# Kernel tuning notes

Hardware: AMD Instinct MI355X
Metric: run time of the kernel (lower is better)

## Reference

```python
import jax, jax.numpy as jnp
import numpy as np

B, C = 8192, 1000
T_KD = 20.0   # KL_divergence temperature
T_TH = 2.0    # Threshold_weights5 temperature
ALPHA = 0.8   # dynamic weight scale


def setup_inputs() -> dict:
    key = jax.random.key(0)
    ks = jax.random.split(key, 7)
    d = {f"outputs{i+1}": jax.random.normal(ks[i], (B, C), jnp.float32) for i in range(5)}
    d["out_s"] = jax.random.normal(ks[5], (B, C), jnp.float32)
    d["targets"] = jax.random.randint(ks[6], (B,), 0, C)
    return d


def _margin(o, targets):
    # per-sample: top1 - top2 if the target class holds the max logit, else 0
    top2 = jax.lax.top_k(o, 2)[0]                                   # [B, 2]
    tgt = jnp.take_along_axis(o, targets[:, None], axis=1)[:, 0]    # [B]
    return jnp.where(tgt == top2[:, 0], top2[:, 0] - top2[:, 1], jnp.zeros_like(tgt))


def reference(outputs1, outputs2, outputs3, outputs4, outputs5, out_s, targets):
    teachers = jnp.stack([outputs1, outputs2, outputs3, outputs4, outputs5], 0)  # [5,B,C]
    mimic = teachers.mean(0)                                                      # [B,C]
    all6 = jnp.concatenate([teachers, mimic[None]], axis=0)                       # [6,B,C]

    # Threshold_weights5: confidence margins -> softmax over the 6 sources
    margins = jax.vmap(lambda o: _margin(o, targets))(all6)        # [6,B]
    out_threshold = jax.nn.softmax(margins / T_TH, axis=0)         # [6,B]
    max_preds = teachers.max()                                     # scalar

    # Calculate_dynamic_weights for each source
    tgt_logits = jnp.take_along_axis(all6, targets[None, :, None], axis=2)[..., 0]  # [6,B]
    w2 = ALPHA * tgt_logits / max_preds                            # [6,B]
    w1 = 1.0 - w2                                                  # [6,B]

    # CE loss (shared across sources) and KD cross-entropy per source
    log_p_s = jax.nn.log_softmax(out_s, axis=1)
    CE = -jnp.take_along_axis(log_p_s, targets[:, None], axis=1)[:, 0]             # [B]
    log_p_sT = jax.nn.log_softmax(out_s / T_KD, axis=1)                            # [B,C]
    p_t = jax.nn.softmax(all6 / T_KD, axis=2)                                      # [6,B,C]
    KD = -jnp.sum(p_t * log_p_sT[None], axis=2) * (T_KD * T_KD)                    # [6,B]

    loss_src = w1 * CE[None, :] + w2 * KD                          # [6,B]
    return jnp.mean(jnp.sum(out_threshold * loss_src, axis=0))
```

## Files before the change

kernel.cpp:

```cpp
#include <hip/hip_runtime.h>
#include <math.h>

#define NROWS 8192
#define NCOLS 1000
#define NB    4096
#define ROWSPB 2
#define NSLOT 64
#define NEGF  -1.0e30f


__device__ __forceinline__ unsigned encf(float x) {
    unsigned u = __float_as_uint(x);
    return (u & 0x80000000u) ? ~u : (u | 0x80000000u);
}
__device__ __forceinline__ float decf(unsigned e) {
    unsigned u = (e & 0x80000000u) ? (e ^ 0x80000000u) : ~e;
    return __uint_as_float(u);
}
__device__ __forceinline__ float pick4(const float* a, int k) {
    return k == 0 ? a[0] : (k == 1 ? a[1] : (k == 2 ? a[2] : a[3]));
}

__global__ __launch_bounds__(64, 4) void row_kernel(
    const float* __restrict__ p0, const float* __restrict__ p1,
    const float* __restrict__ p2, const float* __restrict__ p3,
    const float* __restrict__ p4, const float* __restrict__ p5,
    const int* __restrict__ targets,
    double* __restrict__ S1, double* __restrict__ S2, unsigned* __restrict__ MX)
{
    const int bid = blockIdx.x;
    const int l   = threadIdx.x;

    double accCE = 0.0, accS2 = 0.0;
    float  accMax = NEGF;

    #pragma unroll
    for (int it = 0; it < ROWSPB; ++it) {
        const int row = bid + it * NB;
        const int tgt = targets[row];
        const int t4  = tgt >> 2;
        const int lt  = t4 & 63;
        const int qt  = t4 >> 6;
        const int kt  = tgt & 3;

        float m1[6], m2[6], zs[6], ds[6];
        #pragma unroll
        for (int s = 0; s < 6; ++s) { m1[s] = NEGF; m2[s] = NEGF; zs[s] = 0.f; ds[s] = 0.f; }
        float z1 = 0.f, z20 = 0.f;
        float sg[7];
        #pragma unroll
        for (int s = 0; s < 7; ++s) sg[s] = 0.f;

        #pragma unroll
        for (int q = 0; q < 4; ++q) {
            const int  c4   = l + (q << 6);
            const bool ok   = (c4 < (NCOLS >> 2));
            const size_t base = (size_t)row * NCOLS + ((size_t)c4 << 2);

            float v[7][4];
            if (ok) {
                float4 x0 = *(const float4*)(p0 + base);
                float4 x1 = *(const float4*)(p1 + base);
                float4 x2 = *(const float4*)(p2 + base);
                float4 x3 = *(const float4*)(p3 + base);
                float4 x4 = *(const float4*)(p4 + base);
                float4 x5 = *(const float4*)(p5 + base);
                v[0][0]=x0.x; v[0][1]=x0.y; v[0][2]=x0.z; v[0][3]=x0.w;
                v[1][0]=x1.x; v[1][1]=x1.y; v[1][2]=x1.z; v[1][3]=x1.w;
                v[2][0]=x2.x; v[2][1]=x2.y; v[2][2]=x2.z; v[2][3]=x2.w;
                v[3][0]=x3.x; v[3][1]=x3.y; v[3][2]=x3.z; v[3][3]=x3.w;
                v[4][0]=x4.x; v[4][1]=x4.y; v[4][2]=x4.z; v[4][3]=x4.w;
                v[6][0]=x5.x; v[6][1]=x5.y; v[6][2]=x5.z; v[6][3]=x5.w;
                #pragma unroll
                for (int k = 0; k < 4; ++k)
                    v[5][k] = (v[0][k] + v[1][k] + v[2][k] + v[3][k] + v[4][k]) * 0.2f;
            } else {
                #pragma unroll
                for (int s = 0; s < 7; ++s)
                    #pragma unroll
                    for (int k = 0; k < 4; ++k) v[s][k] = NEGF;
            }

            #pragma unroll
            for (int s = 0; s < 6; ++s) {
                float a = v[s][0], b = v[s][1], c = v[s][2], d = v[s][3];
                float hi1 = fmaxf(a, b), lo1 = fminf(a, b);
                float hi2 = fmaxf(c, d), lo2 = fminf(c, d);
                float q1 = fmaxf(hi1, hi2);
                float q2 = fmaxf(fminf(hi1, hi2), fmaxf(lo1, lo2));
                float nm1 = fmaxf(m1[s], q1);
                float nm2 = fmaxf(fminf(m1[s], q1), fmaxf(m2[s], q2));
                m1[s] = nm1; m2[s] = nm2;
                float zz = 0.f, dot = 0.f;
                #pragma unroll
                for (int k = 0; k < 4; ++k) {
                    float e = __expf(v[s][k] * 0.05f);
                    zz += e; dot += e * v[6][k];
                }
                zs[s] += zz; ds[s] += dot;
            }
            #pragma unroll
            for (int k = 0; k < 4; ++k) {
                z1  += __expf(v[6][k]);
                z20 += __expf(v[6][k] * 0.05f);
            }
            if (ok && q == qt && l == lt) {
                #pragma unroll
                for (int s = 0; s < 7; ++s) sg[s] = pick4(v[s], kt);
            }
        }

        #pragma unroll
        for (int xm = 1; xm < 64; xm <<= 1) {
            #pragma unroll
            for (int s = 0; s < 6; ++s) {
                float o1 = __shfl_xor(m1[s], xm);
                float o2 = __shfl_xor(m2[s], xm);
                float nm1 = fmaxf(m1[s], o1);
                float nm2 = fmaxf(fminf(m1[s], o1), fmaxf(m2[s], o2));
                m1[s] = nm1; m2[s] = nm2;
                zs[s] += __shfl_xor(zs[s], xm);
                ds[s] += __shfl_xor(ds[s], xm);
            }
            z1  += __shfl_xor(z1, xm);
            z20 += __shfl_xor(z20, xm);
        }
        float sgv[7];
        #pragma unroll
        for (int s = 0; s < 7; ++s) sgv[s] = __shfl(sg[s], lt);

        if (l == 0) {
            const float lse1  = logf(z1);
            const float lse20 = logf(z20);
            const float CE    = lse1 - sgv[6];

            float KD[6], mg[6];
            float mmax = 0.f;
            #pragma unroll
            for (int s = 0; s < 6; ++s) {
                KD[s] = 400.f * lse20 - 20.f * (ds[s] / zs[s]);
                mg[s] = (sgv[s] == m1[s]) ? (m1[s] - m2[s]) : 0.f;
                mmax  = fmaxf(mmax, mg[s]);
            }
            float es[6], se = 0.f;
            #pragma unroll
            for (int s = 0; s < 6; ++s) { es[s] = __expf((mg[s] - mmax) * 0.5f); se += es[s]; }

            double rS2 = 0.0;
            #pragma unroll
            for (int s = 0; s < 6; ++s)
                rS2 += (double)(es[s] / se) * (double)sgv[s] * (double)(KD[s] - CE);

            accCE += (double)CE;
            accS2 += rS2;
            float tmax = fmaxf(fmaxf(fmaxf(m1[0], m1[1]), fmaxf(m1[2], m1[3])), m1[4]);
            accMax = fmaxf(accMax, tmax);
        }
    }

    if (l == 0) {
        atomicAdd(&S1[bid & (NSLOT - 1)], accCE);
        atomicAdd(&S2[bid & (NSLOT - 1)], accS2);
        atomicMax(&MX[bid & (NSLOT - 1)], encf(accMax));
    }
}

__global__ void final_kernel(const double* __restrict__ S1, const double* __restrict__ S2,
                             const unsigned* __restrict__ MX, float* __restrict__ out)
{
    const int tid = threadIdx.x;
    double s1 = S1[tid], s2 = S2[tid];
    unsigned m = MX[tid];
    #pragma unroll
    for (int k = 32; k >= 1; k >>= 1) {
        s1 += __shfl_xor(s1, k);
        s2 += __shfl_xor(s2, k);
        unsigned om = __shfl_xor(m, k);
        m = (om > m) ? om : m;
    }
    if (tid == 0) {
        double maxp = (double)decf(m);
        out[0] = (float)((s1 + (0.8 / maxp) * s2) / (double)NROWS);
    }
}

extern "C" void kernel_launch(void* const* d_in, const int* in_sizes, int n_in,
                              void* d_out, int out_size, void* d_ws, size_t ws_size,
                              hipStream_t stream)
{
    const float* t1 = (const float*)d_in[0];
    const float* t2 = (const float*)d_in[1];
    const float* t3 = (const float*)d_in[2];
    const float* t4 = (const float*)d_in[3];
    const float* t5 = (const float*)d_in[4];
    const float* os = (const float*)d_in[5];
    const int* targets = (const int*)d_in[6];

    double*   S1 = (double*)d_ws;
    double*   S2 = S1 + NSLOT;
    unsigned* MX = (unsigned*)(S2 + NSLOT);

    hipMemsetAsync(d_ws, 0, NSLOT * (8 + 8 + 4), stream);
    row_kernel<<<NB, 64, 0, stream>>>(t1, t2, t3, t4, t5, os, targets, S1, S2, MX);
    final_kernel<<<1, 64, 0, stream>>>(S1, S2, MX, (float*)d_out);
}
```

Measured before the change: 227.1 us.

## Use 4-wave blocks with one row per wave instead of looping rows per block

```diff
diff --git a/kernel.cpp b/kernel.cpp
--- a/kernel.cpp
+++ b/kernel.cpp
@@ -3,8 +3,9 @@
 
 #define NROWS 8192
 #define NCOLS 1000
-#define NB    4096
-#define ROWSPB 2
+#define TPB   256
+#define WPB   4
+#define NB    (NROWS / WPB)
 #define NSLOT 64
 #define NEGF  -1.0e30f
 
@@ -21,147 +22,135 @@
     return k == 0 ? a[0] : (k == 1 ? a[1] : (k == 2 ? a[2] : a[3]));
 }
 
-__global__ __launch_bounds__(64, 4) void row_kernel(
+__global__ __launch_bounds__(TPB, 4) void row_kernel(
     const float* __restrict__ p0, const float* __restrict__ p1,
     const float* __restrict__ p2, const float* __restrict__ p3,
     const float* __restrict__ p4, const float* __restrict__ p5,
     const int* __restrict__ targets,
     double* __restrict__ S1, double* __restrict__ S2, unsigned* __restrict__ MX)
 {
-    const int bid = blockIdx.x;
-    const int l   = threadIdx.x;
+    const int wave = threadIdx.x >> 6;
+    const int l    = threadIdx.x & 63;
+    const int row  = blockIdx.x * WPB + wave;
 
-    double accCE = 0.0, accS2 = 0.0;
-    float  accMax = NEGF;
+    const int tgt = targets[row];
+    const int t4  = tgt >> 2;
+    const int lt  = t4 & 63;
+    const int qt  = t4 >> 6;
+    const int kt  = tgt & 3;
 
+    float m1[6], m2[6], zs[6], ds[6];
     #pragma unroll
-    for (int it = 0; it < ROWSPB; ++it) {
-        const int row = bid + it * NB;
-        const int tgt = targets[row];
-        const int t4  = tgt >> 2;
-        const int lt  = t4 & 63;
-        const int qt  = t4 >> 6;
-        const int kt  = tgt & 3;
+    for (int s = 0; s < 6; ++s) { m1[s] = NEGF; m2[s] = NEGF; zs[s] = 0.f; ds[s] = 0.f; }
+    float z1 = 0.f, z20 = 0.f;
+    float sg[7];
+    #pragma unroll
+    for (int s = 0; s < 7; ++s) sg[s] = 0.f;
 
-        float m1[6], m2[6], zs[6], ds[6];
-        #pragma unroll
-        for (int s = 0; s < 6; ++s) { m1[s] = NEGF; m2[s] = NEGF; zs[s] = 0.f; ds[s] = 0.f; }
-        float z1 = 0.f, z20 = 0.f;
-        float sg[7];
-        #pragma unroll
-        for (int s = 0; s < 7; ++s) sg[s] = 0.f;
+    #pragma unroll 2
+    for (int q = 0; q < 4; ++q) {
+        const int  c4 = l + (q << 6);
+        const bool ok = (c4 < (NCOLS >> 2));
+        const size_t base = (size_t)row * NCOLS + ((size_t)c4 << 2);
 
-        #pragma unroll
-        for (int q = 0; q < 4; ++q) {
-            const int  c4   = l + (q << 6);
-            const bool ok   = (c4 < (NCOLS >> 2));
-            const size_t base = (size_t)row * NCOLS + ((size_t)c4 << 2);
-
-            float v[7][4];
-            if (ok) {
-                float4 x0 = *(const float4*)(p0 + base);
-                float4 x1 = *(const float4*)(p1 + base);
-                float4 x2 = *(const float4*)(p2 + base);
-                float4 x3 = *(const float4*)(p3 + base);
-                float4 x4 = *(const float4*)(p4 + base);
-                float4 x5 = *(const float4*)(p5 + base);
-                v[0][0]=x0.x; v[0][1]=x0.y; v[0][2]=x0.z; v[0][3]=x0.w;
-                v[1][0]=x1.x; v[1][1]=x1.y; v[1][2]=x1.z; v[1][3]=x1.w;
-                v[2][0]=x2.x; v[2][1]=x2.y; v[2][2]=x2.z; v[2][3]=x2.w;
-                v[3][0]=x3.x; v[3][1]=x3.y; v[3][2]=x3.z; v[3][3]=x3.w;
-                v[4][0]=x4.x; v[4][1]=x4.y; v[4][2]=x4.z; v[4][3]=x4.w;
-                v[6][0]=x5.x; v[6][1]=x5.y; v[6][2]=x5.z; v[6][3]=x5.w;
+        float v[7][4];
+        if (ok) {
+            float4 x0 = *(const float4*)(p0 + base);
+            float4 x1 = *(const float4*)(p1 + base);
+            float4 x2 = *(const float4*)(p2 + base);
+            float4 x3 = *(const float4*)(p3 + base);
+            float4 x4 = *(const float4*)(p4 + base);
+            float4 x5 = *(const float4*)(p5 + base);
+            v[0][0]=x0.x; v[0][1]=x0.y; v[0][2]=x0.z; v[0][3]=x0.w;
+            v[1][0]=x1.x; v[1][1]=x1.y; v[1][2]=x1.z; v[1][3]=x1.w;
+            v[2][0]=x2.x; v[2][1]=x2.y; v[2][2]=x2.z; v[2][3]=x2.w;
+            v[3][0]=x3.x; v[3][1]=x3.y; v[3][2]=x3.z; v[3][3]=x3.w;
+            v[4][0]=x4.x; v[4][1]=x4.y; v[4][2]=x4.z; v[4][3]=x4.w;
+            v[6][0]=x5.x; v[6][1]=x5.y; v[6][2]=x5.z; v[6][3]=x5.w;
+            #pragma unroll
+            for (int k = 0; k < 4; ++k)
+                v[5][k] = (v[0][k] + v[1][k] + v[2][k] + v[3][k] + v[4][k]) * 0.2f;
+        } else {
+            #pragma unroll
+            for (int s = 0; s < 7; ++s)
                 #pragma unroll
-                for (int k = 0; k < 4; ++k)
-                    v[5][k] = (v[0][k] + v[1][k] + v[2][k] + v[3][k] + v[4][k]) * 0.2f;
-            } else {
-                #pragma unroll
-                for (int s = 0; s < 7; ++s)
-                    #pragma unroll
-                    for (int k = 0; k < 4; ++k) v[s][k] = NEGF;
-            }
-
-            #pragma unroll
-            for (int s = 0; s < 6; ++s) {
-                float a = v[s][0], b = v[s][1], c = v[s][2], d = v[s][3];
-                float hi1 = fmaxf(a, b), lo1 = fminf(a, b);
-                float hi2 = fmaxf(c, d), lo2 = fminf(c, d);
-                float q1 = fmaxf(hi1, hi2);
-                float q2 = fmaxf(fminf(hi1, hi2), fmaxf(lo1, lo2));
-                float nm1 = fmaxf(m1[s], q1);
-                float nm2 = fmaxf(fminf(m1[s], q1), fmaxf(m2[s], q2));
-                m1[s] = nm1; m2[s] = nm2;
-                float zz = 0.f, dot = 0.f;
-                #pragma unroll
-                for (int k = 0; k < 4; ++k) {
-                    float e = __expf(v[s][k] * 0.05f);
-                    zz += e; dot += e * v[6][k];
-                }
-                zs[s] += zz; ds[s] += dot;
-            }
-            #pragma unroll
-            for (int k = 0; k < 4; ++k) {
-                z1  += __expf(v[6][k]);
-                z20 += __expf(v[6][k] * 0.05f);
-            }
-            if (ok && q == qt && l == lt) {
-                #pragma unroll
-                for (int s = 0; s < 7; ++s) sg[s] = pick4(v[s], kt);
-            }
+                for (int k = 0; k < 4; ++k) v[s][k] = NEGF;
         }
 
         #pragma unroll
-        for (int xm = 1; xm < 64; xm <<= 1) {
+        for (int s = 0; s < 6; ++s) {
+            float a = v[s][0], b = v[s][1], c = v[s][2], d = v[s][3];
+            float hi1 = fmaxf(a, b), lo1 = fminf(a, b);
+            float hi2 = fmaxf(c, d), lo2 = fminf(c, d);
+            float q1 = fmaxf(hi1, hi2);
+            float q2 = fmaxf(fminf(hi1, hi2), fmaxf(lo1, lo2));
+            float nm1 = fmaxf(m1[s], q1);
+            float nm2 = fmaxf(fminf(m1[s], q1), fmaxf(m2[s], q2));
+            m1[s] = nm1; m2[s] = nm2;
+            float zz = 0.f, dot = 0.f;
             #pragma unroll
-            for (int s = 0; s < 6; ++s) {
-                float o1 = __shfl_xor(m1[s], xm);
-                float o2 = __shfl_xor(m2[s], xm);
-                float nm1 = fmaxf(m1[s], o1);
-                float nm2 = fmaxf(fminf(m1[s], o1), fmaxf(m2[s], o2));
-                m1[s] = nm1; m2[s] = nm2;
-                zs[s] += __shfl_xor(zs[s], xm);
-                ds[s] += __shfl_xor(ds[s], xm);
+            for (int k = 0; k < 4; ++k) {
+                float e = __expf(v[s][k] * 0.05f);
+                zz += e; dot += e * v[6][k];
             }
-            z1  += __shfl_xor(z1, xm);
-            z20 += __shfl_xor(z20, xm);
+            zs[s] += zz; ds[s] += dot;
         }
-        float sgv[7];
         #pragma unroll
-        for (int s = 0; s < 7; ++s) sgv[s] = __shfl(sg[s], lt);
-
-        if (l == 0) {
-            const float lse1  = logf(z1);
-            const float lse20 = logf(z20);
-            const float CE    = lse1 - sgv[6];
-
-            float KD[6], mg[6];
-            float mmax = 0.f;
+        for (int k = 0; k < 4; ++k) {
+            z1  += __expf(v[6][k]);
+            z20 += __expf(v[6][k] * 0.05f);
+        }
+        if (ok && q == qt && l == lt) {
             #pragma unroll
-            for (int s = 0; s < 6; ++s) {
-                KD[s] = 400.f * lse20 - 20.f * (ds[s] / zs[s]);
-                mg[s] = (sgv[s] == m1[s]) ? (m1[s] - m2[s]) : 0.f;
-                mmax  = fmaxf(mmax, mg[s]);
-            }
-            float es[6], se = 0.f;
-            #pragma unroll
-            for (int s = 0; s < 6; ++s) { es[s] = __expf((mg[s] - mmax) * 0.5f); se += es[s]; }
-
-            double rS2 = 0.0;
-            #pragma unroll
-            for (int s = 0; s < 6; ++s)
-                rS2 += (double)(es[s] / se) * (double)sgv[s] * (double)(KD[s] - CE);
-
-            accCE += (double)CE;
-            accS2 += rS2;
-            float tmax = fmaxf(fmaxf(fmaxf(m1[0], m1[1]), fmaxf(m1[2], m1[3])), m1[4]);
-            accMax = fmaxf(accMax, tmax);
+            for (int s = 0; s < 7; ++s) sg[s] = pick4(v[s], kt);
         }
     }
 
+    #pragma unroll
+    for (int xm = 1; xm < 64; xm <<= 1) {
+        #pragma unroll
+        for (int s = 0; s < 6; ++s) {
+            float o1 = __shfl_xor(m1[s], xm);
+            float o2 = __shfl_xor(m2[s], xm);
+            float nm1 = fmaxf(m1[s], o1);
+            float nm2 = fmaxf(fminf(m1[s], o1), fmaxf(m2[s], o2));
+            m1[s] = nm1; m2[s] = nm2;
+            zs[s] += __shfl_xor(zs[s], xm);
+            ds[s] += __shfl_xor(ds[s], xm);
+        }
+        z1  += __shfl_xor(z1, xm);
+        z20 += __shfl_xor(z20, xm);
+    }
+    float sgv[7];
+    #pragma unroll
+    for (int s = 0; s < 7; ++s) sgv[s] = __shfl(sg[s], lt);
+
     if (l == 0) {
-        atomicAdd(&S1[bid & (NSLOT - 1)], accCE);
-        atomicAdd(&S2[bid & (NSLOT - 1)], accS2);
-        atomicMax(&MX[bid & (NSLOT - 1)], encf(accMax));
+        const float lse1  = logf(z1);
+        const float lse20 = logf(z20);
+        const float CE    = lse1 - sgv[6];
+
+        float KD[6], mg[6];
+        float mmax = 0.f;
+        #pragma unroll
+        for (int s = 0; s < 6; ++s) {
+            KD[s] = 400.f * lse20 - 20.f * (ds[s] / zs[s]);
+            mg[s] = (sgv[s] == m1[s]) ? (m1[s] - m2[s]) : 0.f;
+            mmax  = fmaxf(mmax, mg[s]);
+        }
+        float es[6], se = 0.f;
+        #pragma unroll
+        for (int s = 0; s < 6; ++s) { es[s] = __expf((mg[s] - mmax) * 0.5f); se += es[s]; }
+
+        double rS2 = 0.0;
+        #pragma unroll
+        for (int s = 0; s < 6; ++s)
+            rS2 += (double)(es[s] / se) * (double)sgv[s] * (double)(KD[s] - CE);
+
+        float tmax = fmaxf(fmaxf(fmaxf(m1[0], m1[1]), fmaxf(m1[2], m1[3])), m1[4]);
+        atomicAdd(&S1[row & (NSLOT - 1)], (double)CE);
+        atomicAdd(&S2[row & (NSLOT - 1)], rS2);
+        atomicMax(&MX[row & (NSLOT - 1)], encf(tmax));
     }
 }
 
@@ -201,6 +190,6 @@
     unsigned* MX = (unsigned*)(S2 + NSLOT);
 
     hipMemsetAsync(d_ws, 0, NSLOT * (8 + 8 + 4), stream);
-    row_kernel<<<NB, 64, 0, stream>>>(t1, t2, t3, t4, t5, os, targets, S1, S2, MX);
+    row_kernel<<<NB, TPB, 0, stream>>>(t1, t2, t3, t4, t5, os, targets, S1, S2, MX);
     final_kernel<<<1, 64, 0, stream>>>(S1, S2, MX, (float*)d_out);
 }
```

New measurement: 214.3 us. 1.06x faster.
